# Optimization experiments

Hardware: AMD Instinct MI355X
Metric: run time of the kernel (lower is better)

The kernel has to match this reference:

```python
import jax, jax.numpy as jnp
import numpy as np


def setup_inputs() -> dict:
    key = jax.random.key(0)
    k1, k2, k3 = jax.random.split(key, 3)
    B, S, V, D = 2, 128, 1024, 512
    x = jax.random.normal(k1, (B, S, V, D), dtype=jnp.float32)
    W1 = jax.random.normal(k2, (32, D), dtype=jnp.float32) * (1.0 / np.sqrt(D))
    b1 = jnp.zeros((32,), dtype=jnp.float32)
    W2 = jax.random.normal(k3, (1, 32), dtype=jnp.float32) * (1.0 / np.sqrt(32))
    b2 = jnp.zeros((1,), dtype=jnp.float32)
    return {"x": x, "W1": W1, "b1": b1, "W2": W2, "b2": b2}


def reference(x, W1, b1, W2, b2):
    # x: [B, S, V, D]. Original transposes to [B, V, S, D]; we keep layout and
    # adjust axes, which is the same math.
    h = jnp.einsum('bsvd,kd->bsvk', x, W1) + b1          # [B,S,V,32]
    score = jnp.einsum('bsvk,ok->bsvo', h, W2) + b2      # [B,S,V,1]
    score = score[..., 0]                                # [B,S,V]
    w = jax.nn.softmax(score, axis=1)                    # softmax over seq_len
    out = jnp.einsum('bsv,bsvd->bvd', w, x)              # [B,V,D]
    return out
```

## Files before the change

### kernel.cpp

```cpp
#include <hip/hip_runtime.h>
#include <math.h>


#define BB 2
#define SS 128
#define VV 1024
#define DD 512
#define KK 32
#define WPB 4
#define SW (SS / WPB)

__global__ __launch_bounds__(128) void weff_kernel(
    const float* __restrict__ W1, const float* __restrict__ W2,
    float* __restrict__ weff)
{
    const int d = blockIdx.x * 128 + threadIdx.x;
    float acc = 0.f;
#pragma unroll
    for (int k = 0; k < KK; ++k)
        acc = fmaf(W2[k], W1[k * DD + d], acc);
    weff[d] = acc;
}

__global__ __launch_bounds__(256) void node_attn_kernel(
    const float* __restrict__ x, const float* __restrict__ weff,
    float* __restrict__ out)
{
    const int lane = threadIdx.x & 63;
    const int w    = threadIdx.x >> 6;
    const int pair = blockIdx.x;
    const int b = pair >> 10;
    const int v = pair & (VV - 1);
    const int d0 = lane * 4;
    const int d1 = 256 + lane * 4;

    const float4 wl = *(const float4*)(weff + d0);
    const float4 wh = *(const float4*)(weff + d1);

    const size_t sstr = (size_t)VV * DD;
    const float* xp = x + (size_t)b * SS * sstr + (size_t)v * DD
                        + (size_t)(w * SW) * sstr;

    float4 bl[4], bh[4];
#pragma unroll
    for (int i = 0; i < 4; ++i) {
        bl[i] = *(const float4*)(xp + (size_t)i * sstr + d0);
        bh[i] = *(const float4*)(xp + (size_t)i * sstr + d1);
    }

    float  l  = 0.f;
    float4 ol = make_float4(0.f, 0.f, 0.f, 0.f);
    float4 oh = make_float4(0.f, 0.f, 0.f, 0.f);

    for (int s = 0; s < SW; s += 2) {
        const float4 c0l = bl[s & 3],      c0h = bh[s & 3];
        const float4 c1l = bl[(s + 1) & 3], c1h = bh[(s + 1) & 3];
        if (s + 4 < SW) {
            const float* p0 = xp + (size_t)(s + 4) * sstr;
            const float* p1 = xp + (size_t)(s + 5) * sstr;
            bl[s & 3]       = *(const float4*)(p0 + d0);
            bh[s & 3]       = *(const float4*)(p0 + d1);
            bl[(s + 1) & 3] = *(const float4*)(p1 + d0);
            bh[(s + 1) & 3] = *(const float4*)(p1 + d1);
        }

        float t0 = c0l.x * wl.x + c0l.y * wl.y + c0l.z * wl.z + c0l.w * wl.w
                 + c0h.x * wh.x + c0h.y * wh.y + c0h.z * wh.z + c0h.w * wh.w;
        float t1 = c1l.x * wl.x + c1l.y * wl.y + c1l.z * wl.z + c1l.w * wl.w
                 + c1h.x * wh.x + c1h.y * wh.y + c1h.z * wh.z + c1h.w * wh.w;
#pragma unroll
        for (int off = 32; off > 0; off >>= 1) {
            t0 += __shfl_xor(t0, off, 64);
            t1 += __shfl_xor(t1, off, 64);
        }
        const float p0 = __expf(t0);
        const float p1 = __expf(t1);
        l += p0 + p1;
        ol.x = fmaf(p0, c0l.x, fmaf(p1, c1l.x, ol.x));
        ol.y = fmaf(p0, c0l.y, fmaf(p1, c1l.y, ol.y));
        ol.z = fmaf(p0, c0l.z, fmaf(p1, c1l.z, ol.z));
        ol.w = fmaf(p0, c0l.w, fmaf(p1, c1l.w, ol.w));
        oh.x = fmaf(p0, c0h.x, fmaf(p1, c1h.x, oh.x));
        oh.y = fmaf(p0, c0h.y, fmaf(p1, c1h.y, oh.y));
        oh.z = fmaf(p0, c0h.z, fmaf(p1, c1h.z, oh.z));
        oh.w = fmaf(p0, c0h.w, fmaf(p1, c1h.w, oh.w));
    }

    __shared__ float osh[WPB][DD];
    __shared__ float lsh[WPB];
    *(float4*)(&osh[w][d0]) = ol;
    *(float4*)(&osh[w][d1]) = oh;
    if (lane == 0) lsh[w] = l;
    __syncthreads();

    const int t = threadIdx.x;
    const float lt  = lsh[0] + lsh[1] + lsh[2] + lsh[3];
    const float inv = 1.0f / lt;
    float sx = 0.f, sy = 0.f;
#pragma unroll
    for (int q = 0; q < WPB; ++q) {
        sx += osh[q][t * 2];
        sy += osh[q][t * 2 + 1];
    }
    float* op = out + ((size_t)b * VV + v) * DD;
    *(float2*)(op + t * 2) = make_float2(sx * inv, sy * inv);
}

extern "C" void kernel_launch(void* const* d_in, const int* in_sizes, int n_in,
                              void* d_out, int out_size, void* d_ws, size_t ws_size,
                              hipStream_t stream) {
    const float* x  = (const float*)d_in[0];
    const float* W1 = (const float*)d_in[1];
    const float* W2 = (const float*)d_in[3];
    float* out  = (float*)d_out;
    float* weff = (float*)d_ws;

    weff_kernel<<<dim3(DD / 128), dim3(128), 0, stream>>>(W1, W2, weff);
    node_attn_kernel<<<dim3(BB * VV), dim3(256), 0, stream>>>(x, weff, out);
}
```

Baseline: 687.4 us.

## Process two adjacent V nodes per block with contiguous 4KB row loads

Each block now handles two adjacent nodes (v, v+1), so each sequence step reads a contiguous 4KB span instead of a 2KB span, and the grid is halved to 1024 blocks. Each wave processes one sequence position per iteration for both nodes, with double-buffered prefetch. The shared-memory combine and output store are widened to float4. The aim is better DRAM/cache-line locality and fewer blocks, at the cost of fewer blocks to hide latency and more registers per thread.

```diff
diff --git a/kernel.cpp b/kernel.cpp
--- a/kernel.cpp
+++ b/kernel.cpp
@@ -7,8 +7,7 @@
 #define VV 1024
 #define DD 512
 #define KK 32
-#define WPB 4
-#define SW (SS / WPB)
+#define SW (SS / 4)
 
 __global__ __launch_bounds__(128) void weff_kernel(
     const float* __restrict__ W1, const float* __restrict__ W2,
@@ -27,10 +26,10 @@
     float* __restrict__ out)
 {
     const int lane = threadIdx.x & 63;
-    const int w    = threadIdx.x >> 6;
-    const int pair = blockIdx.x;
-    const int b = pair >> 10;
-    const int v = pair & (VV - 1);
+    const int q    = threadIdx.x >> 6;
+    const int idx  = blockIdx.x;
+    const int b  = idx >> 9;
+    const int v  = (idx & 511) * 2;
     const int d0 = lane * 4;
     const int d1 = 256 + lane * 4;
 
@@ -39,35 +38,36 @@
 
     const size_t sstr = (size_t)VV * DD;
     const float* xp = x + (size_t)b * SS * sstr + (size_t)v * DD
-                        + (size_t)(w * SW) * sstr;
+                        + (size_t)(q * SW) * sstr;
 
-    float4 bl[4], bh[4];
+    float4 b0[2], b1[2], b2[2], b3[2];
 #pragma unroll
-    for (int i = 0; i < 4; ++i) {
-        bl[i] = *(const float4*)(xp + (size_t)i * sstr + d0);
-        bh[i] = *(const float4*)(xp + (size_t)i * sstr + d1);
+    for (int i = 0; i < 2; ++i) {
+        const float* p = xp + (size_t)i * sstr;
+        b0[i] = *(const float4*)(p + d0);
+        b1[i] = *(const float4*)(p + d1);
+        b2[i] = *(const float4*)(p + DD + d0);
+        b3[i] = *(const float4*)(p + DD + d1);
     }
 
-    float  l  = 0.f;
-    float4 ol = make_float4(0.f, 0.f, 0.f, 0.f);
-    float4 oh = make_float4(0.f, 0.f, 0.f, 0.f);
+    float  l0 = 0.f, l1 = 0.f;
+    float4 a0 = make_float4(0.f,0.f,0.f,0.f), a1 = a0, a2 = a0, a3 = a0;
 
-    for (int s = 0; s < SW; s += 2) {
-        const float4 c0l = bl[s & 3],      c0h = bh[s & 3];
-        const float4 c1l = bl[(s + 1) & 3], c1h = bh[(s + 1) & 3];
-        if (s + 4 < SW) {
-            const float* p0 = xp + (size_t)(s + 4) * sstr;
-            const float* p1 = xp + (size_t)(s + 5) * sstr;
-            bl[s & 3]       = *(const float4*)(p0 + d0);
-            bh[s & 3]       = *(const float4*)(p0 + d1);
-            bl[(s + 1) & 3] = *(const float4*)(p1 + d0);
-            bh[(s + 1) & 3] = *(const float4*)(p1 + d1);
+    for (int s = 0; s < SW; ++s) {
+        const float4 c0 = b0[s & 1], c1 = b1[s & 1];
+        const float4 c2 = b2[s & 1], c3 = b3[s & 1];
+        if (s + 2 < SW) {
+            const float* p = xp + (size_t)(s + 2) * sstr;
+            b0[s & 1] = *(const float4*)(p + d0);
+            b1[s & 1] = *(const float4*)(p + d1);
+            b2[s & 1] = *(const float4*)(p + DD + d0);
+            b3[s & 1] = *(const float4*)(p + DD + d1);
         }
 
-        float t0 = c0l.x * wl.x + c0l.y * wl.y + c0l.z * wl.z + c0l.w * wl.w
-                 + c0h.x * wh.x + c0h.y * wh.y + c0h.z * wh.z + c0h.w * wh.w;
-        float t1 = c1l.x * wl.x + c1l.y * wl.y + c1l.z * wl.z + c1l.w * wl.w
-                 + c1h.x * wh.x + c1h.y * wh.y + c1h.z * wh.z + c1h.w * wh.w;
+        float t0 = c0.x*wl.x + c0.y*wl.y + c0.z*wl.z + c0.w*wl.w
+                 + c1.x*wh.x + c1.y*wh.y + c1.z*wh.z + c1.w*wh.w;
+        float t1 = c2.x*wl.x + c2.y*wl.y + c2.z*wl.z + c2.w*wl.w
+                 + c3.x*wh.x + c3.y*wh.y + c3.z*wh.z + c3.w*wh.w;
 #pragma unroll
         for (int off = 32; off > 0; off >>= 1) {
             t0 += __shfl_xor(t0, off, 64);
@@ -75,35 +75,41 @@
         }
         const float p0 = __expf(t0);
         const float p1 = __expf(t1);
-        l += p0 + p1;
-        ol.x = fmaf(p0, c0l.x, fmaf(p1, c1l.x, ol.x));
-        ol.y = fmaf(p0, c0l.y, fmaf(p1, c1l.y, ol.y));
-        ol.z = fmaf(p0, c0l.z, fmaf(p1, c1l.z, ol.z));
-        ol.w = fmaf(p0, c0l.w, fmaf(p1, c1l.w, ol.w));
-        oh.x = fmaf(p0, c0h.x, fmaf(p1, c1h.x, oh.x));
-        oh.y = fmaf(p0, c0h.y, fmaf(p1, c1h.y, oh.y));
-        oh.z = fmaf(p0, c0h.z, fmaf(p1, c1h.z, oh.z));
-        oh.w = fmaf(p0, c0h.w, fmaf(p1, c1h.w, oh.w));
+        l0 += p0;  l1 += p1;
+        a0.x = fmaf(p0, c0.x, a0.x); a0.y = fmaf(p0, c0.y, a0.y);
+        a0.z = fmaf(p0, c0.z, a0.z); a0.w = fmaf(p0, c0.w, a0.w);
+        a1.x = fmaf(p0, c1.x, a1.x); a1.y = fmaf(p0, c1.y, a1.y);
+        a1.z = fmaf(p0, c1.z, a1.z); a1.w = fmaf(p0, c1.w, a1.w);
+        a2.x = fmaf(p1, c2.x, a2.x); a2.y = fmaf(p1, c2.y, a2.y);
+        a2.z = fmaf(p1, c2.z, a2.z); a2.w = fmaf(p1, c2.w, a2.w);
+        a3.x = fmaf(p1, c3.x, a3.x); a3.y = fmaf(p1, c3.y, a3.y);
+        a3.z = fmaf(p1, c3.z, a3.z); a3.w = fmaf(p1, c3.w, a3.w);
     }
 
-    __shared__ float osh[WPB][DD];
-    __shared__ float lsh[WPB];
-    *(float4*)(&osh[w][d0]) = ol;
-    *(float4*)(&osh[w][d1]) = oh;
-    if (lane == 0) lsh[w] = l;
+    __shared__ float osh[4][2][DD];
+    __shared__ float lsh[4][2];
+    *(float4*)(&osh[q][0][d0]) = a0;
+    *(float4*)(&osh[q][0][d1]) = a1;
+    *(float4*)(&osh[q][1][d0]) = a2;
+    *(float4*)(&osh[q][1][d1]) = a3;
+    if (lane == 0) { lsh[q][0] = l0; lsh[q][1] = l1; }
     __syncthreads();
 
-    const int t = threadIdx.x;
-    const float lt  = lsh[0] + lsh[1] + lsh[2] + lsh[3];
+    const int t  = threadIdx.x;
+    const int vl = t >> 7;
+    const int dd = (t & 127) * 4;
+    const float lt  = lsh[0][vl] + lsh[1][vl] + lsh[2][vl] + lsh[3][vl];
     const float inv = 1.0f / lt;
-    float sx = 0.f, sy = 0.f;
-#pragma unroll
-    for (int q = 0; q < WPB; ++q) {
-        sx += osh[q][t * 2];
-        sy += osh[q][t * 2 + 1];
-    }
+    float4 s0 = *(const float4*)(&osh[0][vl][dd]);
+    const float4 s1 = *(const float4*)(&osh[1][vl][dd]);
+    const float4 s2 = *(const float4*)(&osh[2][vl][dd]);
+    const float4 s3 = *(const float4*)(&osh[3][vl][dd]);
+    s0.x = (s0.x + s1.x + s2.x + s3.x) * inv;
+    s0.y = (s0.y + s1.y + s2.y + s3.y) * inv;
+    s0.z = (s0.z + s1.z + s2.z + s3.z) * inv;
+    s0.w = (s0.w + s1.w + s2.w + s3.w) * inv;
     float* op = out + ((size_t)b * VV + v) * DD;
-    *(float2*)(op + t * 2) = make_float2(sx * inv, sy * inv);
+    *(float4*)(op + t * 4) = s0;
 }
 
 extern "C" void kernel_launch(void* const* d_in, const int* in_sizes, int n_in,
@@ -116,5 +122,5 @@
     float* weff = (float*)d_ws;
 
     weff_kernel<<<dim3(DD / 128), dim3(128), 0, stream>>>(W1, W2, weff);
-    node_attn_kernel<<<dim3(BB * VV), dim3(256), 0, stream>>>(x, weff, out);
+    node_attn_kernel<<<dim3(BB * VV / 2), dim3(256), 0, stream>>>(x, weff, out);
 }
```

Measured after the change: 762.3 us. 10.9% more time.
